# Optimization experiments

Measured on AMD Instinct MI355X. Metric: run time of the kernel, lower is better.

Reference implementation:

```python
import jax, jax.numpy as jnp
import numpy as np

N_NODES = 50000
N_EDGES = 800000
IN_C = 16
HID_C = 16
OUT_C = 10
N_GRAPHS = 500
EDGE_DIM = 3
MLP_HID = 25
BN_EPS = 1e-5


def setup_inputs() -> dict:
    key = jax.random.key(0)
    ks = iter(jax.random.split(key, 40))

    def nrm(shape, scale=1.0):
        return jax.random.normal(next(ks), shape, dtype=jnp.float32) * scale

    inp = {}
    inp["x"] = nrm((N_NODES, IN_C))
    inp["edge_index"] = jax.random.randint(next(ks), (2, N_EDGES), 0, N_NODES, dtype=jnp.int32)
    inp["edge_attr"] = jax.random.uniform(next(ks), (N_EDGES, EDGE_DIM), dtype=jnp.float32)
    inp["batch"] = jnp.sort(jax.random.randint(next(ks), (N_NODES,), 0, N_GRAPHS, dtype=jnp.int32))

    def bn_params():
        g = jax.random.uniform(next(ks), (MLP_HID,), minval=0.8, maxval=1.2, dtype=jnp.float32)
        b = nrm((MLP_HID,), 0.1)
        mu = nrm((MLP_HID,), 0.1)
        var = jax.random.uniform(next(ks), (MLP_HID,), minval=0.5, maxval=1.5, dtype=jnp.float32)
        return g, b, mu, var

    # edge MLP 1: 3 -> 25 -> IN_C*HID_C
    inp["W1a"] = nrm((EDGE_DIM, MLP_HID), 0.3)
    inp["b1a"] = nrm((MLP_HID,), 0.05)
    inp["g1"], inp["bt1"], inp["m1"], inp["v1"] = bn_params()
    inp["W1b"] = nrm((MLP_HID, IN_C * HID_C), 0.1)
    inp["b1b"] = nrm((IN_C * HID_C,), 0.05)
    inp["root1"] = nrm((IN_C, HID_C), 0.2)
    inp["bias1"] = nrm((HID_C,), 0.05)

    # edge MLP 2: 3 -> 25 -> HID_C*HID_C
    inp["W2a"] = nrm((EDGE_DIM, MLP_HID), 0.3)
    inp["b2a"] = nrm((MLP_HID,), 0.05)
    inp["g2"], inp["bt2"], inp["m2"], inp["v2"] = bn_params()
    inp["W2b"] = nrm((MLP_HID, HID_C * HID_C), 0.1)
    inp["b2b"] = nrm((HID_C * HID_C,), 0.05)
    inp["root2"] = nrm((HID_C, HID_C), 0.2)
    inp["bias2"] = nrm((HID_C,), 0.05)

    # final MLP([HID_C, OUT_C]) -> single plain linear (plain_last)
    inp["fcW"] = nrm((HID_C, OUT_C), 0.2)
    inp["fcb"] = nrm((OUT_C,), 0.05)
    return inp


def _edge_mlp(e, Wa, ba, g, bt, mu, var, Wb, bb):
    # Linear -> BatchNorm(eval) -> ReLU -> (dropout=eval identity) -> Linear
    h = e @ Wa + ba
    h = g * (h - mu) * jax.lax.rsqrt(var + BN_EPS) + bt
    h = jax.nn.relu(h)
    return h @ Wb + bb


def _nnconv(x, src, dst, w_edge, root, bias, out_dim):
    # message: x_j [E,in] times per-edge weight [E,in,out]
    msg = jnp.einsum("ei,eio->eo", x[src], w_edge)
    agg = jax.ops.segment_sum(msg, dst, num_segments=N_NODES)
    deg = jax.ops.segment_sum(jnp.ones((src.shape[0],), msg.dtype), dst, num_segments=N_NODES)
    agg = agg / jnp.maximum(deg, 1.0)[:, None]  # mean aggregation
    return agg + x @ root + bias


def reference(x, edge_index, edge_attr, batch,
              W1a, b1a, g1, bt1, m1, v1, W1b, b1b, root1, bias1,
              W2a, b2a, g2, bt2, m2, v2, W2b, b2b, root2, bias2,
              fcW, fcb):
    src, dst = edge_index[0], edge_index[1]

    w1 = _edge_mlp(edge_attr, W1a, b1a, g1, bt1, m1, v1, W1b, b1b).reshape(-1, IN_C, HID_C)
    x = jax.nn.elu(_nnconv(x, src, dst, w1, root1, bias1, HID_C))

    w2 = _edge_mlp(edge_attr, W2a, b2a, g2, bt2, m2, v2, W2b, b2b).reshape(-1, HID_C, HID_C)
    x = jax.nn.elu(_nnconv(x, src, dst, w2, root2, bias2, HID_C))

    # global mean pooling over graphs
    pooled = jax.ops.segment_sum(x, batch, num_segments=N_GRAPHS)
    cnt = jax.ops.segment_sum(jnp.ones((x.shape[0],), x.dtype), batch, num_segments=N_GRAPHS)
    pooled = pooled / jnp.maximum(cnt, 1.0)[:, None]

    return pooled @ fcW + fcb  # [N_GRAPHS, OUT_C]
```

## Files before the change

kernel.cpp:

```cpp
#include <hip/hip_runtime.h>
#include <math.h>

#define N_NODES 50000
#define N_EDGES 800000
#define IN_C 16
#define HID_C 16
#define OUT_C 10
#define N_GRAPHS 500
#define EDGE_DIM 3
#define MLP_HID 25
#define BN_EPS 1e-5f

#define SCAN_NB ((N_NODES + 255) / 256)
#define EDGE_NB ((N_EDGES + 255) / 256)

typedef __attribute__((ext_vector_type(8))) _Float16 half8;
typedef __attribute__((ext_vector_type(2))) _Float16 half2v;
typedef __attribute__((ext_vector_type(4))) float f32x4;
union U4H8 { uint4 u; half8 h; half2v p[4]; };
union HU { _Float16 h; unsigned short u; };

__global__ __launch_bounds__(256) void setup_kernel(
    const float* __restrict__ W1a, const float* __restrict__ b1a,
    const float* __restrict__ g1, const float* __restrict__ bt1,
    const float* __restrict__ m1, const float* __restrict__ v1,
    const float* __restrict__ W2a, const float* __restrict__ b2a,
    const float* __restrict__ g2, const float* __restrict__ bt2,
    const float* __restrict__ m2, const float* __restrict__ v2,
    const float* __restrict__ W1b, const float* __restrict__ b1b,
    const float* __restrict__ W2b, const float* __restrict__ b2b,
    const int* __restrict__ batch,
    const float* __restrict__ xin, const float* __restrict__ eattr,
    const int* __restrict__ dst,
    float* __restrict__ AC1, float* __restrict__ AC2,
    unsigned int* __restrict__ WF1, unsigned int* __restrict__ WF2,
    int* __restrict__ goff, int* __restrict__ cnt, int* __restrict__ rank_out,
    float4* __restrict__ ea4, unsigned int* __restrict__ xh0)
{
    const int blk = blockIdx.x;
    const int tid = threadIdx.x;
    if (blk < 7) {
        int t = blk * 256 + tid;
        if (t >= 1664) return;
        const float *Wb, *bb; unsigned int *WH;
        int tl = t;
        if (t < 832) { Wb = W1b; bb = b1b; WH = WF1; }
        else { tl = t - 832; Wb = W2b; bb = b2b; WH = WF2; }
        int m = tl >> 6;
        int L = tl & 63;
        int q = L >> 4, o = L & 15;
        unsigned int hi[8];
        for (int j = 0; j < 8; ++j) {
            int kp = m*32 + q*8 + j;
            int k = kp >> 4, i = kp & 15;
            float w = (k < 25) ? Wb[k*256 + i*16 + o] : bb[i*16 + o];
            HU cv; cv.h = (_Float16)w;
            hi[j] = cv.u;
        }
        int base = (m*64 + L) * 4;
        for (int d = 0; d < 4; ++d)
            WH[base + d] = hi[2*d] | (hi[2*d+1] << 16);
        return;
    }
    if (blk == 7 || blk == 8) {
        if (blk == 7) {
            if (tid < 26) {
                int k = tid;
                if (k < 25) {
                    float sc = g1[k] / sqrtf(v1[k] + BN_EPS);
                    AC1[k*4+0] = sc * W1a[0*MLP_HID+k];
                    AC1[k*4+1] = sc * W1a[1*MLP_HID+k];
                    AC1[k*4+2] = sc * W1a[2*MLP_HID+k];
                    AC1[k*4+3] = sc * (b1a[k] - m1[k]) + bt1[k];
                } else {
                    AC1[100] = 0.f; AC1[101] = 0.f; AC1[102] = 0.f; AC1[103] = 1.f;
                }
            } else if (tid >= 32 && tid < 58) {
                int k = tid - 32;
                if (k < 25) {
                    float sc = g2[k] / sqrtf(v2[k] + BN_EPS);
                    AC2[k*4+0] = sc * W2a[0*MLP_HID+k];
                    AC2[k*4+1] = sc * W2a[1*MLP_HID+k];
                    AC2[k*4+2] = sc * W2a[2*MLP_HID+k];
                    AC2[k*4+3] = sc * (b2a[k] - m2[k]) + bt2[k];
                } else {
                    AC2[100] = 0.f; AC2[101] = 0.f; AC2[102] = 0.f; AC2[103] = 1.f;
                }
            }
        }
        int g = (blk - 7) * 256 + tid;
        if (g <= N_GRAPHS) {
            int lo = 0, hi = N_NODES;
            while (lo < hi) {
                int mid = (lo + hi) >> 1;
                if (batch[mid] < g) lo = mid + 1; else hi = mid;
            }
            goff[g] = lo;
        }
        return;
    }
    const int e = (blk - 9) * 256 + tid;
    if (e < N_EDGES) {
        float4 a;
        a.x = eattr[e*3+0];
        a.y = eattr[e*3+1];
        a.z = eattr[e*3+2];
        a.w = 0.f;
        ea4[e] = a;
        rank_out[e] = atomicAdd(&cnt[dst[e]], 1);
    }
    if (e < 400000) {
        float2 v = ((const float2*)xin)[e];
        HU h0; h0.h = (_Float16)v.x;
        HU h1; h1.h = (_Float16)v.y;
        xh0[e] = (unsigned int)h0.u | ((unsigned int)h1.u << 16);
    }
}

__global__ __launch_bounds__(256) void scan_kernel(
    const int* __restrict__ cnt, int* __restrict__ bsum,
    int* __restrict__ bpre, int* __restrict__ off,
    int* __restrict__ ticket, int* __restrict__ flag)
{
    __shared__ int lds[256];
    __shared__ int sDone;
    int t = threadIdx.x;
    int idx = blockIdx.x * 256 + t;
    int v = (idx < N_NODES) ? cnt[idx] : 0;
    lds[t] = v;
    __syncthreads();
    for (int d = 1; d < 256; d <<= 1) {
        int u = (t >= d) ? lds[t - d] : 0;
        __syncthreads();
        lds[t] += u;
        __syncthreads();
    }
    const int myincl = lds[t];
    const int btot   = lds[255];
    if (t == 0) {
        bsum[blockIdx.x] = btot;
        __threadfence();
        sDone = atomicAdd(ticket, 1);
    }
    __syncthreads();
    if (sDone == SCAN_NB - 1) {
        __threadfence();
        int b = (t < SCAN_NB) ? bsum[t] : 0;
        __syncthreads();
        lds[t] = b;
        __syncthreads();
        for (int d = 1; d < 256; d <<= 1) {
            int u = (t >= d) ? lds[t - d] : 0;
            __syncthreads();
            lds[t] += u;
            __syncthreads();
        }
        if (t < SCAN_NB) bpre[t] = (t > 0) ? lds[t - 1] : 0;
        if (t == 255) off[N_NODES] = lds[255];
        __threadfence();
        if (t == 0)
            __hip_atomic_store(flag, 1, __ATOMIC_RELEASE,
                               __HIP_MEMORY_SCOPE_AGENT);
    } else {
        if (t == 0) {
            while (__hip_atomic_load(flag, __ATOMIC_RELAXED,
                                     __HIP_MEMORY_SCOPE_AGENT) == 0)
                __builtin_amdgcn_s_sleep(2);
            __threadfence();
        }
        __syncthreads();
    }
    if (idx < N_NODES) off[idx] = bpre[blockIdx.x] + myincl - v;
}

__global__ __launch_bounds__(256) void edge_mfma7_kernel(
    const unsigned short* __restrict__ xh,
    const int* __restrict__ src,
    const int* __restrict__ dst,
    const int* __restrict__ rank,
    const int* __restrict__ off,
    const float4* __restrict__ ea4,
    const float* __restrict__ AC,
    const unsigned int* __restrict__ WF,
    float* __restrict__ msg_buf)
{
    __shared__ uint4 wf_s[832];
    const int tid = threadIdx.x;
    #pragma unroll
    for (int it = 0; it < 4; ++it) {
        int gi = tid + it*256;
        if (gi < 832) wf_s[gi] = ((const uint4*)WF)[gi];
    }
    __syncthreads();

    const int wave = tid >> 6;
    const int lane = tid & 63;
    const int q    = lane >> 4;
    const int el   = lane & 15;
    const int i0   = (q & 1) * 8;
    const bool bsel = (q >> 1) != 0;
    const int E0   = (blockIdx.x * 4 + wave) * 64;

    const int sAll = src[E0 + lane];
    const int dAll = dst[E0 + lane];
    const int rAll = rank[E0 + lane];
    const int pAll = off[dAll] + rAll;

    int   sT[4];
    float a0[4], a1[4], a2[4];
    #pragma unroll
    for (int t = 0; t < 4; ++t) {
        sT[t] = __shfl(sAll, t*16 + el);
        float4 at = ea4[E0 + t*16 + el];
        a0[t] = at.x; a1[t] = at.y; a2[t] = at.z;
    }

    U4H8 xf[4];
    #pragma unroll
    for (int t = 0; t < 4; ++t)
        xf[t].u = *(const uint4*)(const void*)(xh + (size_t)sT[t]*16 + i0);

    f32x4 acc0 = {0.f,0.f,0.f,0.f}, acc1 = {0.f,0.f,0.f,0.f};
    f32x4 acc2 = {0.f,0.f,0.f,0.f}, acc3 = {0.f,0.f,0.f,0.f};
    #pragma unroll 1
    for (int m = 0; m < 13; ++m) {
        const float4 Ae = *(const float4*)(AC + m*8);
        const float4 Ao = *(const float4*)(AC + m*8 + 4);
        const float A0 = bsel ? Ao.x : Ae.x;
        const float A1 = bsel ? Ao.y : Ae.y;
        const float A2 = bsel ? Ao.z : Ae.z;
        const float A3 = bsel ? Ao.w : Ae.w;
        U4H8 w; w.u = wf_s[m*64 + lane];
        #pragma unroll
        for (int t = 0; t < 4; ++t) {
            float h = fmaxf(fmaf(a2[t], A2, fmaf(a1[t], A1,
                              fmaf(a0[t], A0, A3))), 0.f);
            _Float16 hh = (_Float16)h;
            half2v h2; h2.x = hh; h2.y = hh;
            U4H8 f;
            #pragma unroll
            for (int j = 0; j < 4; ++j) f.p[j] = h2 * xf[t].p[j];
            f32x4 a = (t==0) ? acc0 : (t==1) ? acc1 : (t==2) ? acc2 : acc3;
            a = __builtin_amdgcn_mfma_f32_16x16x32_f16(w.h, f.h, a, 0, 0, 0);
            if (t==0) acc0 = a; else if (t==1) acc1 = a;
            else if (t==2) acc2 = a; else acc3 = a;
        }
    }

    #pragma unroll
    for (int t = 0; t < 4; ++t) {
        int row = __shfl(pAll, t*16 + el);
        f32x4 a = (t==0) ? acc0 : (t==1) ? acc1 : (t==2) ? acc2 : acc3;
        *(f32x4*)(msg_buf + (size_t)row * HID_C + q*4) = a;
    }
}

__global__ __launch_bounds__(256) void node_gather_kernel(
    const float* __restrict__ xin, const float* __restrict__ msg_buf,
    const int* __restrict__ off,
    const float* __restrict__ root, const float* __restrict__ bias,
    float* __restrict__ xout, unsigned int* __restrict__ xh_out)
{
    __shared__ float root_s[IN_C * HID_C];
    if (threadIdx.x < 64)
        ((float4*)root_s)[threadIdx.x] = ((const float4*)root)[threadIdx.x];
    __syncthreads();

    int t = blockIdx.x * blockDim.x + threadIdx.x;
    int n = t >> 2;
    if (n >= N_NODES) return;
    int c0 = (t & 3) * 4;
    int lo = off[n], hi = off[n+1];
    float inv = 1.f / fmaxf((float)(hi - lo), 1.f);

    const f32x4* m4 = (const f32x4*)msg_buf;
    const int qi = c0 >> 2;
    f32x4 s0 = {0.f,0.f,0.f,0.f}, s1 = {0.f,0.f,0.f,0.f};
    int r = lo;
    for (; r + 2 <= hi; r += 2) {
        s0 += m4[(size_t)r*4 + qi];
        s1 += m4[(size_t)(r+1)*4 + qi];
    }
    if (r < hi) s0 += m4[(size_t)r*4 + qi];
    f32x4 s = s0 + s1;

    const float4 bv = *(const float4*)(bias + c0);
    f32x4 acc;
    acc.x = fmaf(s.x, inv, bv.x);
    acc.y = fmaf(s.y, inv, bv.y);
    acc.z = fmaf(s.z, inv, bv.z);
    acc.w = fmaf(s.w, inv, bv.w);

    const float4* x4 = (const float4*)(xin + (size_t)n * IN_C);
    #pragma unroll
    for (int j = 0; j < 4; ++j) {
        float4 xv = x4[j];
        #pragma unroll
        for (int k = 0; k < 4; ++k) {
            float xi = (k==0) ? xv.x : (k==1) ? xv.y : (k==2) ? xv.z : xv.w;
            const float4 rv = *(const float4*)(root_s + (j*4+k)*HID_C + c0);
            acc.x = fmaf(xi, rv.x, acc.x);
            acc.y = fmaf(xi, rv.y, acc.y);
            acc.z = fmaf(xi, rv.z, acc.z);
            acc.w = fmaf(xi, rv.w, acc.w);
        }
    }

    acc.x = acc.x > 0.f ? acc.x : (expf(acc.x) - 1.f);
    acc.y = acc.y > 0.f ? acc.y : (expf(acc.y) - 1.f);
    acc.z = acc.z > 0.f ? acc.z : (expf(acc.z) - 1.f);
    acc.w = acc.w > 0.f ? acc.w : (expf(acc.w) - 1.f);
    *(f32x4*)(xout + (size_t)n * HID_C + c0) = acc;

    if (xh_out) {
        HU h0, h1, h2, h3;
        h0.h = (_Float16)acc.x; h1.h = (_Float16)acc.y;
        h2.h = (_Float16)acc.z; h3.h = (_Float16)acc.w;
        uint2 pk;
        pk.x = (unsigned int)h0.u | ((unsigned int)h1.u << 16);
        pk.y = (unsigned int)h2.u | ((unsigned int)h3.u << 16);
        ((uint2*)xh_out)[n*4 + qi] = pk;
    }
}

__global__ __launch_bounds__(64) void pool_final_kernel(
    const float* __restrict__ xin, const int* __restrict__ goff,
    const float* __restrict__ fcW, const float* __restrict__ fcb,
    float* __restrict__ out)
{
    __shared__ float part[4][HID_C];
    __shared__ float pooled[HID_C];
    int g = blockIdx.x;
    int t = threadIdx.x;
    int c = t & 15, sub = t >> 4;
    int lo = goff[g], hi = goff[g+1];
    float s = 0.f;
    for (int n = lo + sub; n < hi; n += 4)
        s += xin[(size_t)n*HID_C + c];
    part[sub][c] = s;
    __syncthreads();
    if (t < HID_C) {
        pooled[t] = (part[0][t] + part[1][t] + part[2][t] + part[3][t])
                    / fmaxf((float)(hi - lo), 1.f);
    }
    __syncthreads();
    if (t < OUT_C) {
        float acc = fcb[t];
        #pragma unroll
        for (int i = 0; i < HID_C; ++i)
            acc = fmaf(pooled[i], fcW[i*OUT_C+t], acc);
        out[g*OUT_C + t] = acc;
    }
}


extern "C" void kernel_launch(void* const* d_in, const int* in_sizes, int n_in,
                              void* d_out, int out_size, void* d_ws, size_t ws_size,
                              hipStream_t stream)
{
    const float* x     = (const float*)d_in[0];
    const int*   ei    = (const int*)d_in[1];
    const float* eattr = (const float*)d_in[2];
    const int*   batch = (const int*)d_in[3];
    const float* W1a   = (const float*)d_in[4];
    const float* b1a   = (const float*)d_in[5];
    const float* g1    = (const float*)d_in[6];
    const float* bt1   = (const float*)d_in[7];
    const float* m1    = (const float*)d_in[8];
    const float* v1    = (const float*)d_in[9];
    const float* W1b   = (const float*)d_in[10];
    const float* b1b   = (const float*)d_in[11];
    const float* root1 = (const float*)d_in[12];
    const float* bias1 = (const float*)d_in[13];
    const float* W2a   = (const float*)d_in[14];
    const float* b2a   = (const float*)d_in[15];
    const float* g2    = (const float*)d_in[16];
    const float* bt2   = (const float*)d_in[17];
    const float* m2    = (const float*)d_in[18];
    const float* v2    = (const float*)d_in[19];
    const float* W2b   = (const float*)d_in[20];
    const float* b2b   = (const float*)d_in[21];
    const float* root2 = (const float*)d_in[22];
    const float* bias2 = (const float*)d_in[23];
    const float* fcW   = (const float*)d_in[24];
    const float* fcb   = (const float*)d_in[25];

    const int* src = ei;
    const int* dst = ei + N_EDGES;

    float* ws   = (float*)d_ws;
    float* MSG  = ws;
    float* X1   = ws + 12800000;
    float* X2   = ws + 13600000;
    int*   RANK = (int*)(ws + 14400000);
    int*   CNT  = (int*)(ws + 15200000);
    int*   TICK = (int*)(ws + 15250000);
    int*   FLAG = (int*)(ws + 15250001);
    int*   OFF  = (int*)(ws + 15250016);
    int*   GOFF = (int*)(ws + 15300064);
    unsigned int* WF1 = (unsigned int*)(ws + 15300576);
    unsigned int* WF2 = (unsigned int*)(ws + 15303904);
    float* AC1  = ws + 15307232;
    float* AC2  = ws + 15307344;
    int*   BSUM = (int*)(ws + 15307456);
    int*   BPRE = (int*)(ws + 15307712);
    float* EA4  = ws + 15308032;
    unsigned int* XH0 = (unsigned int*)(ws + 18508032);
    unsigned int* XH1 = (unsigned int*)(ws + 18908032);

    hipMemsetAsync(CNT, 0, 50016 * sizeof(int), stream);

    setup_kernel<<<9 + EDGE_NB, 256, 0, stream>>>(
        W1a, b1a, g1, bt1, m1, v1, W2a, b2a, g2, bt2, m2, v2,
        W1b, b1b, W2b, b2b, batch, x, eattr, dst,
        AC1, AC2, WF1, WF2, GOFF, CNT, RANK, (float4*)EA4, XH0);
    scan_kernel<<<SCAN_NB, 256, 0, stream>>>(CNT, BSUM, BPRE, OFF, TICK, FLAG);

    edge_mfma7_kernel<<<N_EDGES/256, 256, 0, stream>>>(
        (const unsigned short*)XH0, src, dst, RANK, OFF,
        (const float4*)EA4, AC1, WF1, MSG);
    node_gather_kernel<<<(N_NODES*4 + 255)/256, 256, 0, stream>>>(
        x, MSG, OFF, root1, bias1, X1, XH1);

    edge_mfma7_kernel<<<N_EDGES/256, 256, 0, stream>>>(
        (const unsigned short*)XH1, src, dst, RANK, OFF,
        (const float4*)EA4, AC2, WF2, MSG);
    node_gather_kernel<<<(N_NODES*4 + 255)/256, 256, 0, stream>>>(
        X1, MSG, OFF, root2, bias2, X2, (unsigned int*)nullptr);

    pool_final_kernel<<<N_GRAPHS, 64, 0, stream>>>(X2, GOFF, fcW, fcb, (float*)d_out);
}
```

Measured before the change: 254.7 us.

## Split node gather across 16 threads per node with shuffle reduction

The node gather kernel now assigns 16 threads per node instead of 4: each group of four lanes takes an interleaved quarter of the incoming message rows and a quarter of the root matmul. Partial sums are combined with xor shuffles, and one lane per column quad applies the bias, ELU and stores. The aim is more parallelism and memory-level concurrency for the variable-length CSR row sums, which helps hide latency on high-degree nodes. The cost is four times as many threads, extra shuffles, and idle lanes in the epilogue. The bounds check was dropped, which is safe only because 50000*16 divides evenly by 256.

```diff
diff --git a/kernel.cpp b/kernel.cpp
--- a/kernel.cpp
+++ b/kernel.cpp
@@ -267,59 +267,66 @@
     __syncthreads();
 
     int t = blockIdx.x * blockDim.x + threadIdx.x;
-    int n = t >> 2;
-    if (n >= N_NODES) return;
-    int c0 = (t & 3) * 4;
+    int n  = t >> 4;
+    int sub = t & 15;
+    int qi = sub & 3;
+    int h  = sub >> 2;
     int lo = off[n], hi = off[n+1];
     float inv = 1.f / fmaxf((float)(hi - lo), 1.f);
 
     const f32x4* m4 = (const f32x4*)msg_buf;
-    const int qi = c0 >> 2;
     f32x4 s0 = {0.f,0.f,0.f,0.f}, s1 = {0.f,0.f,0.f,0.f};
-    int r = lo;
-    for (; r + 2 <= hi; r += 2) {
+    int r = lo + h;
+    for (; r + 4 < hi; r += 8) {
         s0 += m4[(size_t)r*4 + qi];
-        s1 += m4[(size_t)(r+1)*4 + qi];
+        s1 += m4[(size_t)(r+4)*4 + qi];
     }
     if (r < hi) s0 += m4[(size_t)r*4 + qi];
-    f32x4 s = s0 + s1;
-
-    const float4 bv = *(const float4*)(bias + c0);
-    f32x4 acc;
-    acc.x = fmaf(s.x, inv, bv.x);
-    acc.y = fmaf(s.y, inv, bv.y);
-    acc.z = fmaf(s.z, inv, bv.z);
-    acc.w = fmaf(s.w, inv, bv.w);
-
-    const float4* x4 = (const float4*)(xin + (size_t)n * IN_C);
-    #pragma unroll
-    for (int j = 0; j < 4; ++j) {
-        float4 xv = x4[j];
-        #pragma unroll
-        for (int k = 0; k < 4; ++k) {
-            float xi = (k==0) ? xv.x : (k==1) ? xv.y : (k==2) ? xv.z : xv.w;
-            const float4 rv = *(const float4*)(root_s + (j*4+k)*HID_C + c0);
-            acc.x = fmaf(xi, rv.x, acc.x);
-            acc.y = fmaf(xi, rv.y, acc.y);
-            acc.z = fmaf(xi, rv.z, acc.z);
-            acc.w = fmaf(xi, rv.w, acc.w);
-        }
-    }
-
-    acc.x = acc.x > 0.f ? acc.x : (expf(acc.x) - 1.f);
-    acc.y = acc.y > 0.f ? acc.y : (expf(acc.y) - 1.f);
-    acc.z = acc.z > 0.f ? acc.z : (expf(acc.z) - 1.f);
-    acc.w = acc.w > 0.f ? acc.w : (expf(acc.w) - 1.f);
-    *(f32x4*)(xout + (size_t)n * HID_C + c0) = acc;
-
-    if (xh_out) {
-        HU h0, h1, h2, h3;
-        h0.h = (_Float16)acc.x; h1.h = (_Float16)acc.y;
-        h2.h = (_Float16)acc.z; h3.h = (_Float16)acc.w;
-        uint2 pk;
-        pk.x = (unsigned int)h0.u | ((unsigned int)h1.u << 16);
-        pk.y = (unsigned int)h2.u | ((unsigned int)h3.u << 16);
-        ((uint2*)xh_out)[n*4 + qi] = pk;
+    f32x4 p = s0 + s1;
+    p.x *= inv; p.y *= inv; p.z *= inv; p.w *= inv;
+
+    const float4 xv = ((const float4*)(xin + (size_t)n * IN_C))[h];
+    #pragma unroll
+    for (int k = 0; k < 4; ++k) {
+        float xi = (k==0) ? xv.x : (k==1) ? xv.y : (k==2) ? xv.z : xv.w;
+        const float4 rv = *(const float4*)(root_s + (h*4+k)*HID_C + qi*4);
+        p.x = fmaf(xi, rv.x, p.x);
+        p.y = fmaf(xi, rv.y, p.y);
+        p.z = fmaf(xi, rv.z, p.z);
+        p.w = fmaf(xi, rv.w, p.w);
+    }
+
+    #pragma unroll
+    for (int mask = 4; mask <= 8; mask <<= 1) {
+        p.x += __shfl_xor(p.x, mask);
+        p.y += __shfl_xor(p.y, mask);
+        p.z += __shfl_xor(p.z, mask);
+        p.w += __shfl_xor(p.w, mask);
+    }
+
+    if (h == 0) {
+        const int c0 = qi * 4;
+        const float4 bv = *(const float4*)(bias + c0);
+        f32x4 acc;
+        acc.x = p.x + bv.x;
+        acc.y = p.y + bv.y;
+        acc.z = p.z + bv.z;
+        acc.w = p.w + bv.w;
+        acc.x = acc.x > 0.f ? acc.x : (expf(acc.x) - 1.f);
+        acc.y = acc.y > 0.f ? acc.y : (expf(acc.y) - 1.f);
+        acc.z = acc.z > 0.f ? acc.z : (expf(acc.z) - 1.f);
+        acc.w = acc.w > 0.f ? acc.w : (expf(acc.w) - 1.f);
+        *(f32x4*)(xout + (size_t)n * HID_C + c0) = acc;
+
+        if (xh_out) {
+            HU h0, h1, h2, h3;
+            h0.h = (_Float16)acc.x; h1.h = (_Float16)acc.y;
+            h2.h = (_Float16)acc.z; h3.h = (_Float16)acc.w;
+            uint2 pk;
+            pk.x = (unsigned int)h0.u | ((unsigned int)h1.u << 16);
+            pk.y = (unsigned int)h2.u | ((unsigned int)h3.u << 16);
+            ((uint2*)xh_out)[n*4 + qi] = pk;
+        }
     }
 }
 
@@ -419,13 +426,13 @@
     edge_mfma7_kernel<<<N_EDGES/256, 256, 0, stream>>>(
         (const unsigned short*)XH0, src, dst, RANK, OFF,
         (const float4*)EA4, AC1, WF1, MSG);
-    node_gather_kernel<<<(N_NODES*4 + 255)/256, 256, 0, stream>>>(
+    node_gather_kernel<<<(N_NODES*16)/256, 256, 0, stream>>>(
         x, MSG, OFF, root1, bias1, X1, XH1);
 
     edge_mfma7_kernel<<<N_EDGES/256, 256, 0, stream>>>(
         (const unsigned short*)XH1, src, dst, RANK, OFF,
         (const float4*)EA4, AC2, WF2, MSG);
-    node_gather_kernel<<<(N_NODES*4 + 255)/256, 256, 0, stream>>>(
+    node_gather_kernel<<<(N_NODES*16)/256, 256, 0, stream>>>(
         X1, MSG, OFF, root2, bias2, X2, (unsigned int*)nullptr);
 
     pool_final_kernel<<<N_GRAPHS, 64, 0, stream>>>(X2, GOFF, fcW, fcb, (float*)d_out);
```

After: 252.8 us. About the same (-0.7%).
